# Performance work log

Measured on AMD Instinct MI355X. Metric: run time of the kernel, lower is better.

The kernel has to match this reference:

```python
import jax, jax.numpy as jnp
import numpy as np
import math

B, C, T = 4, 512, 2048
LN_EPS = 1e-5

def setup_inputs() -> dict:
    key = jax.random.key(0)
    ks = jax.random.split(key, 12)
    s = 1.0 / math.sqrt(C)
    inp = {
        'feat': jax.random.normal(ks[0], (B, C, T), dtype=jnp.float32),
        'Wq': jax.random.normal(ks[1], (C, C), dtype=jnp.float32) * s,
        'bq': jax.random.normal(ks[2], (C,), dtype=jnp.float32) * s,
        'Wk': jax.random.normal(ks[3], (C, C), dtype=jnp.float32) * s,
        'bk': jax.random.normal(ks[4], (C,), dtype=jnp.float32) * s,
        'Wv': jax.random.normal(ks[5], (C, C), dtype=jnp.float32) * s,
        'bv': jax.random.normal(ks[6], (C,), dtype=jnp.float32) * s,
        'Ws': jax.random.normal(ks[7], (C, C), dtype=jnp.float32) * s,
        'bs': jax.random.normal(ks[8], (C,), dtype=jnp.float32) * s,
        'Wl': jax.random.normal(ks[9], (C,), dtype=jnp.float32) * s,
        'bl': jax.random.normal(ks[10], (1,), dtype=jnp.float32) * s,
    }
    return inp

def reference(feat, Wq, bq, Wk, bk, Wv, bv, Ws, bs, Wl, bl):
    d = feat.shape[1]
    # 1x1 Conv1d == per-position linear over channels. feat: [B,C,T]
    value = jnp.einsum('oc,bct->bto', Wv, feat) + bv          # [B,T,C]
    query = jnp.einsum('oc,bct->bto', Wq, feat) + bq          # [B,T,C]
    key_  = jnp.einsum('oc,bct->bct', Wk, feat) + bk[:, None] # [B,C,T]
    f = jnp.einsum('btc,bcs->bts', query, key_) / math.sqrt(d)
    f = jax.nn.softmax(f, axis=2)                             # [B,T,T]
    y = jnp.einsum('bts,bsc->btc', f, value)                  # [B,T,C]
    f_score = jax.nn.sigmoid(jnp.einsum('btc,c->bt', y, Wl) + bl[0])
    z = jnp.einsum('bts,bsc->btc', 1.0 - f, value)            # [B,T,C]
    b_score = 1.0 - jax.nn.sigmoid(jnp.einsum('btc,c->bt', z, Wl) + bl[0])
    f_score = (f_score + b_score) / 2.0
    y_ct = jnp.einsum('oc,btc->bot', Ws, y) + bs[:, None]     # smooth conv, [B,C,T]
    out = feat + y_ct
    # LayerNorm over (C, T) jointly, default affine (weight=1, bias=0)
    mu = jnp.mean(out, axis=(1, 2), keepdims=True)
    var = jnp.mean(jnp.square(out - mu), axis=(1, 2), keepdims=True)
    out = (out - mu) * jax.lax.rsqrt(var + LN_EPS)
    return out, f_score
```

## Files before the change

kernel.cpp:

```cpp
#include <hip/hip_runtime.h>
#include <hip/hip_bf16.h>

#define BB 4
#define CC 512
#define TT 2048
static constexpr long CT  = (long)CC * TT;
static constexpr long TC  = (long)TT * CC;
static constexpr long TTT = (long)TT * TT;
static constexpr float SM_SCALE = 0.04419417382415922f;

typedef __bf16 bf16;
typedef __attribute__((ext_vector_type(8))) __bf16 bf16x8;
typedef __attribute__((ext_vector_type(4))) __bf16 bf16x4;
typedef __attribute__((ext_vector_type(4))) float f32x4;

__device__ __forceinline__ void load_lds16(const bf16* g, bf16* l)
{
    __builtin_amdgcn_global_load_lds(
        (const __attribute__((address_space(1))) void*)g,
        (__attribute__((address_space(3))) void*)l, 16, 0, 0);
}

#define FENCE asm volatile("" ::: "memory")

template <int N> __device__ __forceinline__ void vm_wait()
{
    if constexpr (N == 0)       asm volatile("s_waitcnt vmcnt(0)" ::: "memory");
    else if constexpr (N == 4)  asm volatile("s_waitcnt vmcnt(4)" ::: "memory");
    else if constexpr (N == 5)  asm volatile("s_waitcnt vmcnt(5)" ::: "memory");
    else if constexpr (N == 8)  asm volatile("s_waitcnt vmcnt(8)" ::: "memory");
    else if constexpr (N == 10) asm volatile("s_waitcnt vmcnt(10)" ::: "memory");
    else static_assert(N == 0, "unsupported vmcnt literal");
}

template <int TM, int TN, int WR, int WC, int BK, int DEPTH>
struct CorePipe {
    static constexpr int THREADS = WR * WC * 64;
    static constexpr int MI = TM / (WR * 16);
    static constexpr int NI = TN / (WC * 16);
    static constexpr int CPR = BK / 8;
    static constexpr int RSH = (BK == 64) ? 3 : 2;
    static constexpr int CMASK = CPR - 1;
    static constexpr int CHUNKS = (TM + TN) * CPR;
    static constexpr int ACH = TM * CPR;
    static constexpr int CPT = CHUNKS / THREADS;
    static_assert(CPT * THREADS == CHUNKS, "chunk divisibility");
    static_assert(DEPTH == 2 || DEPTH == 3, "depth 2 or 3");

    __device__ static __forceinline__ void stage(
        const bf16* __restrict__ Ab, const bf16* __restrict__ Bb,
        int K, int m0, int n0, int t, int p, bf16* As, bf16* Bs, int tid)
    {
#pragma unroll
        for (int i = 0; i < CPT; ++i) {
            int c = tid + i * THREADS;
            if (c < ACH) {
                int row = c >> RSH;
                int gc  = (c & CMASK) ^ (row & CMASK);
                load_lds16(Ab + (long)(m0 + row) * K + t * BK + gc * 8,
                           As + p * (TM * BK) + c * 8);
            } else {
                int d = c - ACH;
                int row = d >> RSH;
                int gc  = (d & CMASK) ^ (row & CMASK);
                load_lds16(Bb + (long)(n0 + row) * K + t * BK + gc * 8,
                           Bs + p * (TN * BK) + d * 8);
            }
        }
    }

    __device__ static __forceinline__ void run(
        const bf16* __restrict__ Ab, const bf16* __restrict__ Bb,
        int K, int m0, int n0, bf16* As, bf16* Bs, f32x4 (&acc)[MI][NI])
    {
        const int tid  = threadIdx.x;
        const int lane = tid & 63;
        const int wid  = tid >> 6;
        const int wr = (wid / WC) * (MI * 16);
        const int wc = (wid % WC) * (NI * 16);
        const int lm = lane & 15;
        const int lq = lane >> 4;
        const int nt = K / BK;

#pragma unroll
        for (int d = 0; d < DEPTH; ++d)
            stage(Ab, Bb, K, m0, n0, d, d, As, Bs, tid);
        vm_wait<CPT * (DEPTH - 1)>();
        FENCE; __builtin_amdgcn_s_barrier(); FENCE;

        int p = 0;
        for (int t = 0; t < nt; ++t) {
            const bf16* Ap = As + p * (TM * BK);
            const bf16* Bp = Bs + p * (TN * BK);
            bf16x8 af[BK / 32][MI], bfr[BK / 32][NI];
#pragma unroll
            for (int ks = 0; ks < BK / 32; ++ks) {
#pragma unroll
                for (int i = 0; i < MI; ++i) {
                    int ar = wr + i * 16 + lm;
                    int cc = (ks * 4 + lq) ^ (ar & CMASK);
                    af[ks][i] = *(const bf16x8*)(Ap + ar * BK + cc * 8);
                }
#pragma unroll
                for (int i = 0; i < NI; ++i) {
                    int br = wc + i * 16 + lm;
                    int cc = (ks * 4 + lq) ^ (br & CMASK);
                    bfr[ks][i] = *(const bf16x8*)(Bp + br * BK + cc * 8);
                }
            }
            asm volatile("s_waitcnt lgkmcnt(0)" ::: "memory");
            __builtin_amdgcn_sched_barrier(0);
            FENCE; __builtin_amdgcn_s_barrier(); FENCE;
            if (t + DEPTH < nt)
                stage(Ab, Bb, K, m0, n0, t + DEPTH, p, As, Bs, tid);
            __builtin_amdgcn_s_setprio(1);
#pragma unroll
            for (int ks = 0; ks < BK / 32; ++ks)
#pragma unroll
                for (int mi = 0; mi < MI; ++mi)
#pragma unroll
                    for (int ni = 0; ni < NI; ++ni)
                        acc[mi][ni] = __builtin_amdgcn_mfma_f32_16x16x32_bf16(
                            af[ks][mi], bfr[ks][ni], acc[mi][ni], 0, 0, 0);
            __builtin_amdgcn_s_setprio(0);
            if (t + 1 < nt) {
                const int rem = nt - t;
                if (rem > DEPTH)                    vm_wait<CPT * (DEPTH - 1)>();
                else if (DEPTH == 3 && rem == 3)    vm_wait<CPT>();
                else                                vm_wait<0>();
                FENCE; __builtin_amdgcn_s_barrier(); FENCE;
            }
            p = (p + 1 == DEPTH) ? 0 : p + 1;
        }
    }
};

using CPVS  = CorePipe<128, 128, 4, 2, 64, 2>;
using CPOUT = CorePipe<64, 256, 1, 8, 64, 2>;

struct CoreQVPipe {
    static constexpr int THREADS = 512;
    static constexpr int MI = 2;
    static constexpr int NI = 4;
    static constexpr int BK = 64;
    static constexpr int CPR = 8, RSH = 3, CMASK = 7;
    static constexpr int ACH = 128 * 8;
    static constexpr int CHUNKS = 256 * 8;
    static constexpr int CPT = CHUNKS / THREADS;

    __device__ static __forceinline__ void stage(
        const bf16* __restrict__ Ab, const bf16* __restrict__ Bq,
        const bf16* __restrict__ Bv, int m0, int t, int p,
        bf16* As, bf16* Bs, int tid)
    {
#pragma unroll
        for (int i = 0; i < CPT; ++i) {
            int c = tid + i * THREADS;
            if (c < ACH) {
                int row = c >> RSH;
                int gc  = (c & CMASK) ^ (row & CMASK);
                load_lds16(Ab + (long)(m0 + row) * 512 + t * 64 + gc * 8,
                           As + p * (128 * 64) + c * 8);
            } else {
                int d = c - ACH;
                int row = d >> RSH;
                int gc  = (d & CMASK) ^ (row & CMASK);
                const bf16* src = (row < 64)
                    ? Bq + (long)row * 512
                    : Bv + (long)(row - 64) * 512;
                load_lds16(src + t * 64 + gc * 8, Bs + p * (128 * 64) + d * 8);
            }
        }
    }

    __device__ static __forceinline__ void run(
        const bf16* __restrict__ Ab, const bf16* __restrict__ Bq,
        const bf16* __restrict__ Bv,
        int m0, bf16* As, bf16* Bs, f32x4 (&acc)[MI][NI])
    {
        const int tid  = threadIdx.x;
        const int lane = tid & 63;
        const int wid  = tid >> 6;
        const int wr = (wid / 2) * 32;
        const int wc = (wid % 2) * 64;
        const int lm = lane & 15;
        const int lq = lane >> 4;
        const int nt = 8;

        stage(Ab, Bq, Bv, m0, 0, 0, As, Bs, tid);
        stage(Ab, Bq, Bv, m0, 1, 1, As, Bs, tid);
        vm_wait<4>();
        FENCE; __builtin_amdgcn_s_barrier(); FENCE;

        for (int t = 0; t < nt; ++t) {
            const int p = t & 1;
            const bf16* Ap = As + p * (128 * 64);
            const bf16* Bp = Bs + p * (128 * 64);
            bf16x8 af[2][MI], bfr[2][NI];
#pragma unroll
            for (int ks = 0; ks < 2; ++ks) {
#pragma unroll
                for (int i = 0; i < MI; ++i) {
                    int ar = wr + i * 16 + lm;
                    int cc = (ks * 4 + lq) ^ (ar & CMASK);
                    af[ks][i] = *(const bf16x8*)(Ap + ar * BK + cc * 8);
                }
#pragma unroll
                for (int i = 0; i < NI; ++i) {
                    int br = wc + i * 16 + lm;
                    int cc = (ks * 4 + lq) ^ (br & CMASK);
                    bfr[ks][i] = *(const bf16x8*)(Bp + br * BK + cc * 8);
                }
            }
            asm volatile("s_waitcnt lgkmcnt(0)" ::: "memory");
            __builtin_amdgcn_sched_barrier(0);
            FENCE; __builtin_amdgcn_s_barrier(); FENCE;
            if (t + 2 < nt)
                stage(Ab, Bq, Bv, m0, t + 2, p, As, Bs, tid);
            __builtin_amdgcn_s_setprio(1);
#pragma unroll
            for (int ks = 0; ks < 2; ++ks)
#pragma unroll
                for (int mi = 0; mi < MI; ++mi)
#pragma unroll
                    for (int ni = 0; ni < NI; ++ni)
                        acc[mi][ni] = __builtin_amdgcn_mfma_f32_16x16x32_bf16(
                            af[ks][mi], bfr[ks][ni], acc[mi][ni], 0, 0, 0);
            __builtin_amdgcn_s_setprio(0);
            if (t + 1 < nt) {
                if (t + 2 < nt) vm_wait<4>();
                else            vm_wait<0>();
                FENCE; __builtin_amdgcn_s_barrier(); FENCE;
            }
        }
    }
};

__global__ __launch_bounds__(512)
void gemm_qv_kernel(const bf16* __restrict__ featT, const bf16* __restrict__ Wq_bf,
                    const bf16* __restrict__ Wv_bf, bf16* __restrict__ Qb,
                    bf16* __restrict__ Vn, const float* __restrict__ bq,
                    const float* __restrict__ bv, const float* __restrict__ wkc,
                    const float* __restrict__ bk, float* __restrict__ qb,
                    const float* __restrict__ Wl, float* __restrict__ vl)
{
    __shared__ __align__(16) bf16 As[2 * 128 * 64];
    __shared__ __align__(16) bf16 Bs[2 * 128 * 64];
    const int rb = blockIdx.z;
    const int m0 = blockIdx.y * 128;
    const int ng = blockIdx.x;
    const long wofs = (long)(ng * 64) * 512;
    f32x4 acc[2][4] = {};
    CoreQVPipe::run(featT + (long)rb * TC, Wq_bf + wofs, Wv_bf + wofs, m0, As, Bs, acc);

    const int lane = threadIdx.x & 63, wid = threadIdx.x >> 6;
    const int wr = (wid / 2) * 32;
    const bool isV = wid & 1;
    const int lm = lane & 15, lq = lane >> 4;

    if (isV) {
        bf16* outV = Vn + (long)rb * TC;
        float* vlb = vl + (long)rb * TT;
        float vs_[2][4] = {};
#pragma unroll
        for (int mi = 0; mi < 2; ++mi)
#pragma unroll
            for (int ni = 0; ni < 4; ++ni) {
                int n = ng * 64 + ni * 16 + lm;
                float bn = bv[n], wn = Wl[n];
#pragma unroll
                for (int r = 0; r < 4; ++r) {
                    int m = m0 + wr + mi * 16 + lq * 4 + r;
                    float v = acc[mi][ni][r] + bn;
                    outV[(long)m * 512 + n] = (bf16)v;
                    vs_[mi][r] += v * wn;
                }
            }
#pragma unroll
        for (int mi = 0; mi < 2; ++mi)
#pragma unroll
            for (int r = 0; r < 4; ++r) {
                float s = vs_[mi][r];
                s += __shfl_xor(s, 1, 64); s += __shfl_xor(s, 2, 64);
                s += __shfl_xor(s, 4, 64); s += __shfl_xor(s, 8, 64);
                if (lm == 0)
                    atomicAdd(vlb + m0 + wr + mi * 16 + lq * 4 + r, s);
            }
    } else {
        bf16* out = Qb + (long)rb * TC;
        float* qbb = qb + (long)rb * TT;
        float rs[2][4] = {};
#pragma unroll
        for (int mi = 0; mi < 2; ++mi)
#pragma unroll
            for (int ni = 0; ni < 4; ++ni) {
                int n = ng * 64 + ni * 16 + lm;
                float bn = bq[n], wn = wkc[n], kn = bk[n];
#pragma unroll
                for (int r = 0; r < 4; ++r) {
                    int m = m0 + wr + mi * 16 + lq * 4 + r;
                    float v = acc[mi][ni][r] + bn;
                    rs[mi][r] += v * kn;
                    out[(long)m * 512 + n] = (bf16)(v * wn);
                }
            }
#pragma unroll
        for (int mi = 0; mi < 2; ++mi)
#pragma unroll
            for (int r = 0; r < 4; ++r) {
                float s = rs[mi][r];
                s += __shfl_xor(s, 1, 64); s += __shfl_xor(s, 2, 64);
                s += __shfl_xor(s, 4, 64); s += __shfl_xor(s, 8, 64);
                if (lm == 0)
                    atomicAdd(qbb + m0 + wr + mi * 16 + lq * 4 + r, s);
            }
    }
}

__global__ __launch_bounds__(512, 2)
void gemm_mid_kernel(const bf16* __restrict__ Qb, const bf16* __restrict__ featT,
                     bf16* __restrict__ S, const float* __restrict__ qb,
                     float* __restrict__ rsum, const float* __restrict__ vl,
                     float* __restrict__ u, const bf16* __restrict__ Vn,
                     const bf16* __restrict__ Ws_bf, bf16* __restrict__ Vpt)
{
    __shared__ __align__(16) bf16 lds[2][2][256 * 64];
    const int tid  = threadIdx.x;
    const int lane = tid & 63;
    const int wid  = tid >> 6;
    const int lm = lane & 15, lq = lane >> 4;

    if (blockIdx.x >= 256) {
        const int id2 = blockIdx.x - 256;
        const int xcd = id2 & 7, s = id2 >> 3;
        const int bz = xcd >> 1;
        const int m0 = (((xcd & 1) << 1) + (s >> 4)) * 128;
        const int n0 = (s & 15) * 128;
        bf16* As = &lds[0][0][0];
        bf16* Bs = &lds[0][1][0];
        f32x4 acc[2][4] = {};
        CPVS::run(Ws_bf, Vn + (long)bz * TC, 512, m0, n0, As, Bs, acc);

        const int wr = (wid / 2) * 32, wc = (wid % 2) * 64;
        bf16* outp = Vpt + (long)bz * CT;
#pragma unroll
        for (int mi = 0; mi < 2; ++mi)
#pragma unroll
            for (int ni = 0; ni < 4; ++ni) {
                int n = n0 + wc + ni * 16 + lm;
#pragma unroll
                for (int r = 0; r < 4; ++r) {
                    int m = m0 + wr + mi * 16 + lq * 4 + r;
                    outp[(long)m * 2048 + n] = (bf16)acc[mi][ni][r];
                }
            }
        return;
    }

    const int id   = blockIdx.x;
    const int xcd  = id & 7, sIdx = id >> 3;
    const int bz   = xcd >> 1;
    const int n0   = (sIdx & 7) * 256;
    const int m0   = (((xcd & 1) << 2) + (sIdx >> 3)) * 256;
    const bf16* __restrict__ Ab = Qb + (long)bz * TC;
    const bf16* __restrict__ Bb = featT + (long)bz * TC;

    const int wrb = (wid >> 2) * 64;
    const int wcb = (wid & 3) * 32;

    f32x4 acc[8][4] = {};

#define STAGE_HT(t, op, h)                                                    \
    do {                                                                      \
        const bf16* gp_ = (op) ? Bb : Ab;                                     \
        const int  br_  = ((op) ? n0 : m0) + (h) * 128;                       \
        bf16* lp_ = &lds[(t) & 1][op][(h) * 128 * 64];                        \
        _Pragma("unroll")                                                     \
        for (int i_ = 0; i_ < 2; ++i_) {                                      \
            int c_ = tid + i_ * 512;                                          \
            int r_ = c_ >> 3;                                                 \
            int g_ = (c_ & 7) ^ (r_ & 7);                                     \
            load_lds16(gp_ + (long)(br_ + r_) * 512 + (t) * 64 + g_ * 8,      \
                       lp_ + c_ * 8);                                         \
        }                                                                     \
    } while (0)

#define PHASE(t, qm, qn, doSt, st, sop, sh, doVm)                             \
    do {                                                                      \
        bf16x8 af[2][4], bfr[2][2];                                           \
        const bf16* Al_ = lds[(t) & 1][0];                                    \
        const bf16* Bl_ = lds[(t) & 1][1];                                    \
        _Pragma("unroll")                                                     \
        for (int ks = 0; ks < 2; ++ks) {                                      \
            _Pragma("unroll")                                                 \
            for (int j = 0; j < 4; ++j) {                                     \
                int ar = (qm) * 128 + wrb + j * 16 + lm;                      \
                int cc = (ks * 4 + lq) ^ (ar & 7);                            \
                af[ks][j] = *(const bf16x8*)(Al_ + ar * 64 + cc * 8);         \
            }                                                                 \
            _Pragma("unroll")                                                 \
            for (int j = 0; j < 2; ++j) {                                     \
                int br = (qn) * 128 + wcb + j * 16 + lm;                      \
                int cc = (ks * 4 + lq) ^ (br & 7);                            \
                bfr[ks][j] = *(const bf16x8*)(Bl_ + br * 64 + cc * 8);        \
            }                                                                 \
        }                                                                     \
        if (doSt) STAGE_HT(st, sop, sh);                                      \
        if (doVm) {                                                           \
            if ((t) < 6) asm volatile("s_waitcnt vmcnt(4)" ::: "memory");     \
            else         asm volatile("s_waitcnt vmcnt(0)" ::: "memory");     \
        }                                                                     \
        FENCE; __builtin_amdgcn_s_barrier(); FENCE;                           \
        __builtin_amdgcn_s_setprio(1);                                        \
        _Pragma("unroll")                                                     \
        for (int ks = 0; ks < 2; ++ks)                                        \
            _Pragma("unroll")                                                 \
            for (int j = 0; j < 4; ++j)                                       \
                _Pragma("unroll")                                             \
                for (int j2 = 0; j2 < 2; ++j2)                                \
                    acc[(qm) * 4 + j][(qn) * 2 + j2] =                        \
                        __builtin_amdgcn_mfma_f32_16x16x32_bf16(              \
                            af[ks][j], bfr[ks][j2],                           \
                            acc[(qm) * 4 + j][(qn) * 2 + j2], 0, 0, 0);       \
        __builtin_amdgcn_s_setprio(0);                                        \
        FENCE; __builtin_amdgcn_s_barrier(); FENCE;                           \
    } while (0)

    STAGE_HT(0, 0, 0); STAGE_HT(0, 1, 0); STAGE_HT(0, 0, 1); STAGE_HT(0, 1, 1);
    STAGE_HT(1, 0, 0); STAGE_HT(1, 1, 0);
    asm volatile("s_waitcnt vmcnt(4)" ::: "memory");
    FENCE; __builtin_amdgcn_s_barrier(); FENCE;

    for (int t = 0; t < 8; ++t) {
        PHASE(t, 0, 0, t + 1 < 8, t + 1, 0, 1, false);
        PHASE(t, 0, 1, t + 1 < 8, t + 1, 1, 1, false);
        PHASE(t, 1, 0, t + 2 < 8, t + 2, 0, 0, false);
        PHASE(t, 1, 1, t + 2 < 8, t + 2, 1, 0, true);
    }
#undef PHASE
#undef STAGE_HT

    bf16* outp = S + (long)bz * TTT;
    const float* qbb = qb + (long)bz * TT;
    const float* vlb = vl + (long)bz * TT;
    float* rsb = rsum + (long)bz * TT;
    float* ub  = u + (long)bz * TT;
#pragma unroll
    for (int mi = 0; mi < 8; ++mi) {
        const int mrow = m0 + (mi >> 2) * 128 + wrb + (mi & 3) * 16 + lq * 4;
        const f32x4 qv = *(const f32x4*)(qbb + mrow);
        float rp[4] = {0.f, 0.f, 0.f, 0.f};
        float up[4] = {0.f, 0.f, 0.f, 0.f};
#pragma unroll
        for (int ni = 0; ni < 4; ++ni) {
            const int ncol = n0 + (ni >> 1) * 128 + wcb + (ni & 1) * 16 + lm;
            const float vlv = vlb[ncol];
#pragma unroll
            for (int r = 0; r < 4; ++r) {
                float p = __expf((acc[mi][ni][r] + qv[r]) * SM_SCALE);
                outp[(long)(mrow + r) * 2048 + ncol] = (bf16)p;
                rp[r] += p;
                up[r] += p * vlv;
            }
        }
#pragma unroll
        for (int r = 0; r < 4; ++r) {
            float s2 = rp[r], s3 = up[r];
            s2 += __shfl_xor(s2, 1, 64); s2 += __shfl_xor(s2, 2, 64);
            s2 += __shfl_xor(s2, 4, 64); s2 += __shfl_xor(s2, 8, 64);
            s3 += __shfl_xor(s3, 1, 64); s3 += __shfl_xor(s3, 2, 64);
            s3 += __shfl_xor(s3, 4, 64); s3 += __shfl_xor(s3, 8, 64);
            if (lm == 0) {
                atomicAdd(rsb + mrow + r, s2);
                atomicAdd(ub + mrow + r, s3);
            }
        }
    }
}

__global__ __launch_bounds__(512)
void gemm_out_kernel(const bf16* __restrict__ S, const bf16* __restrict__ Vpt,
                     float* __restrict__ out, const float* __restrict__ bs,
                     const float* __restrict__ feat,
                     const float* __restrict__ rsum, double* __restrict__ stats)
{
    __shared__ __align__(16) bf16 As[2 * 64 * 64];
    __shared__ __align__(16) bf16 Bs[2 * 256 * 64];
    __shared__ float red[16];
    const int id = blockIdx.x;
    const int xcd = id & 7, sIdx = id >> 3;
    const int bz = xcd >> 1;
    const int n0 = (sIdx & 1) * 256;
    const int m0 = (((xcd & 1) << 4) + (sIdx >> 1)) * 64;
    f32x4 acc[4][2] = {};
    CPOUT::run(S + (long)bz * TTT, Vpt + (long)bz * CT, 2048, m0, n0, As, Bs, acc);

    const int tid = threadIdx.x;
    const int lane = tid & 63, wid = tid >> 6;
    const int lm = lane & 15, lq = lane >> 4;
    const float* rsb = rsum + (long)bz * TT;
    float inv[4][4];
#pragma unroll
    for (int mi = 0; mi < 4; ++mi) {
        int mrow = m0 + mi * 16 + lq * 4;
        f32x4 rv = *(const f32x4*)(rsb + mrow);
#pragma unroll
        for (int r = 0; r < 4; ++r) inv[mi][r] = 1.f / rv[r];
    }
    float s1 = 0.f, s2 = 0.f;
#pragma unroll
    for (int mi = 0; mi < 4; ++mi)
#pragma unroll
        for (int ni = 0; ni < 2; ++ni) {
            int mrow = m0 + mi * 16 + lq * 4;
            int n = n0 + wid * 32 + ni * 16 + lm;
            long off = (long)bz * CT + (long)n * TT + mrow;
            f32x4 fv = *(const f32x4*)(feat + off);
            float bn = bs[n];
            f32x4 res;
#pragma unroll
            for (int r = 0; r < 4; ++r) {
                float v = acc[mi][ni][r] * inv[mi][r] + bn + fv[r];
                res[r] = v;
                s1 += v;
                s2 += v * v;
            }
            *(f32x4*)(out + off) = res;
        }
#pragma unroll
    for (int off = 32; off; off >>= 1) {
        s1 += __shfl_xor(s1, off, 64);
        s2 += __shfl_xor(s2, off, 64);
    }
    if (lane == 0) { red[wid] = s1; red[8 + wid] = s2; }
    __syncthreads();
    if (tid == 0) {
        double t1 = 0.0, t2 = 0.0;
#pragma unroll
        for (int w = 0; w < 8; ++w) { t1 += red[w]; t2 += red[8 + w]; }
        atomicAdd(stats + bz * 2, t1);
        atomicAdd(stats + bz * 2 + 1, t2);
    }
}

__global__ __launch_bounds__(256)
void prep_kernel(const float* __restrict__ feat, bf16* __restrict__ featT,
                 const float* __restrict__ Wq, const float* __restrict__ Wv,
                 const float* __restrict__ Ws, bf16* __restrict__ Wbf,
                 const float* __restrict__ Wk, const float* __restrict__ Wl,
                 const float* __restrict__ bv, float* __restrict__ wkc,
                 float* __restrict__ wvl, float* __restrict__ wlbv,
                 float* __restrict__ frp, float* __restrict__ qb,
                 float* __restrict__ u, float* __restrict__ rsum,
                 double* __restrict__ stats, float* __restrict__ vl)
{
    const int blk = blockIdx.x;
    const int tid = threadIdx.x;
    if (blk < 4096) {
        __shared__ float tile[32][33];
        __shared__ float sfr[4][32];
        const int b  = blk >> 10;
        const int c0 = ((blk & 1023) >> 6) * 32;
        const int tt = blk & 63;
        const int t0 = tt * 32;
        const int tx = tid & 31;
        const int ty = tid >> 5;
#pragma unroll
        for (int j = 0; j < 4; ++j) {
            int c = c0 + ty + j * 8;
            tile[ty + j * 8][tx] = feat[(long)b * CT + (long)c * TT + t0 + tx];
        }
        __syncthreads();
        float ps = 0.f;
#pragma unroll
        for (int j = 0; j < 4; ++j) {
            int tl = ty + j * 8;
            int t = t0 + tl;
            int c = c0 + tx;
            float v = tile[tx][tl];
            ps += v;
            featT[(long)b * TC + (long)t * CC + c] = (bf16)v;
        }
        const int wid = tid >> 6;
        ps += __shfl_xor(ps, 32, 64);
        if ((tid & 63) < 32) sfr[wid][tx] = ps;
        __syncthreads();
        if (tid < 32) {
            float s = sfr[0][tid] + sfr[1][tid] + sfr[2][tid] + sfr[3][tid];
            frp[(((long)b * 64 + tt) << 9) + c0 + tid] = s;
        }
    } else if (blk < 4480) {
        long gid = (long)(blk - 4096) * 256 + tid;
        long idx = gid * 8;
        int w = (int)(idx >> 18);
        long off = idx & 262143;
        const float* src = (w == 0) ? Wq : (w == 1) ? Wv : Ws;
        f32x4 a = *(const f32x4*)(src + off);
        f32x4 b = *(const f32x4*)(src + off + 4);
        bf16x8 o;
#pragma unroll
        for (int j = 0; j < 4; ++j) { o[j] = (bf16)a[j]; o[4 + j] = (bf16)b[j]; }
        *(bf16x8*)(Wbf + idx) = o;
    } else {
        int mid = (blk - 4480) * 256 + tid;
        if (mid < 512) {
            float s = 0.f;
            for (int o = 0; o < 512; ++o) s += Wk[o * 512 + mid];
            wkc[mid] = s;
        } else if (mid < 1024) {
            int k = mid - 512;
            float s = 0.f;
            for (int c = 0; c < 512; ++c) s += Wl[c] * Wv[c * 512 + k];
            wvl[k] = s;
        } else if (mid < 1088) {
            int lane = mid - 1024;
            float s = 0.f;
#pragma unroll
            for (int j = 0; j < 8; ++j) s += Wl[lane + 64 * j] * bv[lane + 64 * j];
#pragma unroll
            for (int off = 32; off; off >>= 1) s += __shfl_xor(s, off, 64);
            if (lane == 0) wlbv[0] = s;
        } else if (mid >= 1152 && mid < 1160) {
            stats[mid - 1152] = 0.0;
        } else if (mid >= 4096 && mid < 12288) {
            qb[mid - 4096] = 0.f;
        } else if (mid >= 12288 && mid < 20480) {
            u[mid - 12288] = 0.f;
        } else if (mid >= 20480 && mid < 28672) {
            rsum[mid - 20480] = 0.f;
        } else if (mid >= 28672 && mid < 36864) {
            vl[mid - 28672] = 0.f;
        }
    }
}

__global__ __launch_bounds__(256)
void ln_score_kernel(float* __restrict__ out, const double* __restrict__ stats,
                     const float* __restrict__ u, const float* __restrict__ frp,
                     const float* __restrict__ wvl, const float* __restrict__ wlbv,
                     const float* __restrict__ blp, const float* __restrict__ rsum)
{
    if (blockIdx.x < 4096) {
        long i = ((long)blockIdx.x * 256 + threadIdx.x) * 4;
        int b = (int)(i >> 20);
        const double n = 1048576.0;
        double mu  = stats[b * 2] / n;
        double var = stats[b * 2 + 1] / n - mu * mu;
        float rs = (float)(1.0 / sqrt(var + 1e-5));
        float muf = (float)mu;
        f32x4 v = *(f32x4*)(out + i);
#pragma unroll
        for (int j = 0; j < 4; ++j) v[j] = (v[j] - muf) * rs;
        *(f32x4*)(out + i) = v;
    } else {
        const int b = blockIdx.x - 4096;
        __shared__ float ssv[4];
        const int tid = threadIdx.x, lane = tid & 63, wid = tid >> 6;
        const float* fb = frp + ((long)b * 64 << 9);
        float s0 = 0.f, s1 = 0.f;
#pragma unroll 8
        for (int k = 0; k < 64; ++k) {
            s0 += fb[(k << 9) + tid];
            s1 += fb[(k << 9) + tid + 256];
        }
        float p = s0 * wvl[tid] + s1 * wvl[tid + 256];
#pragma unroll
        for (int off = 32; off; off >>= 1) p += __shfl_xor(p, off, 64);
        if (lane == 0) ssv[wid] = p;
        __syncthreads();
        const float sv = ssv[0] + ssv[1] + ssv[2] + ssv[3] + 2048.f * wlbv[0];
        const float bl0 = blp[0];
#pragma unroll
        for (int j = 0; j < 8; ++j) {
            int t = tid + j * 256;
            float uu = u[(long)b * TT + t] / rsum[(long)b * TT + t];
            float uf = uu + bl0;
            float vf = sv - uu + bl0;
            float fs  = 1.f / (1.f + __expf(-uf));
            float bsc = 1.f - 1.f / (1.f + __expf(-vf));
            out[(long)BB * CT + (long)b * TT + t] = 0.5f * (fs + bsc);
        }
    }
}

extern "C" void kernel_launch(void* const* d_in, const int* in_sizes, int n_in,
                              void* d_out, int out_size, void* d_ws, size_t ws_size,
                              hipStream_t stream)
{
    const float* feat = (const float*)d_in[0];
    const float* Wq   = (const float*)d_in[1];
    const float* bq   = (const float*)d_in[2];
    const float* Wk   = (const float*)d_in[3];
    const float* bk   = (const float*)d_in[4];
    const float* Wv   = (const float*)d_in[5];
    const float* bv   = (const float*)d_in[6];
    const float* Ws   = (const float*)d_in[7];
    const float* bs   = (const float*)d_in[8];
    const float* Wl   = (const float*)d_in[9];
    const float* bl   = (const float*)d_in[10];
    float* out = (float*)d_out;

    if (ws_size < 69349504) return;
    char* ws = (char*)d_ws;
    bf16* featT  = (bf16*)(ws);
    bf16* Wbf    = (bf16*)(ws + 8388608);
    bf16* Qb     = (bf16*)(ws + 9961472);
    bf16* Vn     = (bf16*)(ws + 18350080);
    bf16* Vpt    = (bf16*)(ws + 26738688);
    bf16* S      = (bf16*)(ws + 35127296);
    float* wkc   = (float*)(ws + 68689920);
    float* wvl   = (float*)(ws + 68691968);
    float* wlbv  = (float*)(ws + 68694016);
    float* qb    = (float*)(ws + 68694080);
    double* stats= (double*)(ws + 68726848);
    float* u     = (float*)(ws + 68726912);
    float* rsum  = (float*)(ws + 68759680);
    float* frp   = (float*)(ws + 68792448);
    float* vl    = (float*)(ws + 69316736);

    bf16* Wq_bf = Wbf;
    bf16* Wv_bf = Wbf + 262144;
    bf16* Ws_bf = Wbf + 524288;

    prep_kernel<<<4624, 256, 0, stream>>>(feat, featT, Wq, Wv, Ws, Wbf, Wk, Wl, bv,
                                          wkc, wvl, wlbv, frp, qb, u, rsum, stats, vl);
    gemm_qv_kernel<<<dim3(8, 16, 4), 512, 0, stream>>>(
        featT, Wq_bf, Wv_bf, Qb, Vn, bq, bv, wkc, bk, qb, Wl, vl);
    gemm_mid_kernel<<<512, 512, 0, stream>>>(Qb, featT, S, qb, rsum, vl, u,
                                             Vn, Ws_bf, Vpt);
    gemm_out_kernel<<<256, 512, 0, stream>>>(S, Vpt, out, bs, feat, rsum, stats);
    ln_score_kernel<<<4100, 256, 0, stream>>>(out, stats, u, frp, wvl, wlbv, bl, rsum);
}
```

Baseline: 212.1 us.

## Fold Ws into Wv so V projection directly yields Ws·V, dropping the per-batch GEMM

Precomputes the weight product Ws·Wv (and bias Ws·bv) in a small new kernel, so the QV projection writes the smoothed value tensor Vpt directly instead of producing V and then running a separate Ws×V GEMM per batch inside the middle kernel. The vl vector (Wl·V) is now computed from featT with the precomputed Wl·Wv vector instead of atomics in the QV epilogue. This removes a batch-sized GEMM and the V intermediate at the cost of an extra launch and an extra bf16 rounding of the fused weight.

```diff
diff --git a/kernel.cpp b/kernel.cpp
--- a/kernel.cpp
+++ b/kernel.cpp
@@ -25,27 +25,25 @@
 
 template <int N> __device__ __forceinline__ void vm_wait()
 {
-    if constexpr (N == 0)       asm volatile("s_waitcnt vmcnt(0)" ::: "memory");
-    else if constexpr (N == 4)  asm volatile("s_waitcnt vmcnt(4)" ::: "memory");
-    else if constexpr (N == 5)  asm volatile("s_waitcnt vmcnt(5)" ::: "memory");
-    else if constexpr (N == 8)  asm volatile("s_waitcnt vmcnt(8)" ::: "memory");
-    else if constexpr (N == 10) asm volatile("s_waitcnt vmcnt(10)" ::: "memory");
+    if constexpr (N == 0)      asm volatile("s_waitcnt vmcnt(0)" ::: "memory");
+    else if constexpr (N == 3) asm volatile("s_waitcnt vmcnt(3)" ::: "memory");
+    else if constexpr (N == 4) asm volatile("s_waitcnt vmcnt(4)" ::: "memory");
+    else if constexpr (N == 5) asm volatile("s_waitcnt vmcnt(5)" ::: "memory");
     else static_assert(N == 0, "unsupported vmcnt literal");
 }
 
-template <int TM, int TN, int WR, int WC, int BK, int DEPTH>
+template <int TM, int TN, int WR, int WC, int BK>
 struct CorePipe {
     static constexpr int THREADS = WR * WC * 64;
     static constexpr int MI = TM / (WR * 16);
     static constexpr int NI = TN / (WC * 16);
     static constexpr int CPR = BK / 8;
-    static constexpr int RSH = (BK == 64) ? 3 : 2;
+    static constexpr int RSH = 3;
     static constexpr int CMASK = CPR - 1;
     static constexpr int CHUNKS = (TM + TN) * CPR;
     static constexpr int ACH = TM * CPR;
     static constexpr int CPT = CHUNKS / THREADS;
     static_assert(CPT * THREADS == CHUNKS, "chunk divisibility");
-    static_assert(DEPTH == 2 || DEPTH == 3, "depth 2 or 3");
 
     __device__ static __forceinline__ void stage(
         const bf16* __restrict__ Ab, const bf16* __restrict__ Bb,
@@ -82,14 +80,13 @@
         const int lq = lane >> 4;
         const int nt = K / BK;
 
-#pragma unroll
-        for (int d = 0; d < DEPTH; ++d)
-            stage(Ab, Bb, K, m0, n0, d, d, As, Bs, tid);
-        vm_wait<CPT * (DEPTH - 1)>();
+        stage(Ab, Bb, K, m0, n0, 0, 0, As, Bs, tid);
+        stage(Ab, Bb, K, m0, n0, 1, 1, As, Bs, tid);
+        vm_wait<CPT>();
         FENCE; __builtin_amdgcn_s_barrier(); FENCE;
 
-        int p = 0;
         for (int t = 0; t < nt; ++t) {
+            const int p = t & 1;
             const bf16* Ap = As + p * (TM * BK);
             const bf16* Bp = Bs + p * (TN * BK);
             bf16x8 af[BK / 32][MI], bfr[BK / 32][NI];
@@ -111,8 +108,8 @@
             asm volatile("s_waitcnt lgkmcnt(0)" ::: "memory");
             __builtin_amdgcn_sched_barrier(0);
             FENCE; __builtin_amdgcn_s_barrier(); FENCE;
-            if (t + DEPTH < nt)
-                stage(Ab, Bb, K, m0, n0, t + DEPTH, p, As, Bs, tid);
+            if (t + 2 < nt)
+                stage(Ab, Bb, K, m0, n0, t + 2, p, As, Bs, tid);
             __builtin_amdgcn_s_setprio(1);
 #pragma unroll
             for (int ks = 0; ks < BK / 32; ++ks)
@@ -124,29 +121,19 @@
                             af[ks][mi], bfr[ks][ni], acc[mi][ni], 0, 0, 0);
             __builtin_amdgcn_s_setprio(0);
             if (t + 1 < nt) {
-                const int rem = nt - t;
-                if (rem > DEPTH)                    vm_wait<CPT * (DEPTH - 1)>();
-                else if (DEPTH == 3 && rem == 3)    vm_wait<CPT>();
-                else                                vm_wait<0>();
+                if (t + 2 < nt) vm_wait<CPT>();
+                else            vm_wait<0>();
                 FENCE; __builtin_amdgcn_s_barrier(); FENCE;
             }
-            p = (p + 1 == DEPTH) ? 0 : p + 1;
         }
     }
 };
 
-using CPVS  = CorePipe<128, 128, 4, 2, 64, 2>;
-using CPOUT = CorePipe<64, 256, 1, 8, 64, 2>;
+using CW    = CorePipe<128, 64, 4, 2, 64>;
+using CPOUT = CorePipe<64, 256, 1, 8, 64>;
 
 struct CoreQVPipe {
-    static constexpr int THREADS = 512;
-    static constexpr int MI = 2;
-    static constexpr int NI = 4;
-    static constexpr int BK = 64;
-    static constexpr int CPR = 8, RSH = 3, CMASK = 7;
     static constexpr int ACH = 128 * 8;
-    static constexpr int CHUNKS = 256 * 8;
-    static constexpr int CPT = CHUNKS / THREADS;
 
     __device__ static __forceinline__ void stage(
         const bf16* __restrict__ Ab, const bf16* __restrict__ Bq,
@@ -154,17 +141,17 @@
         bf16* As, bf16* Bs, int tid)
     {
 #pragma unroll
-        for (int i = 0; i < CPT; ++i) {
-            int c = tid + i * THREADS;
+        for (int i = 0; i < 4; ++i) {
+            int c = tid + i * 512;
             if (c < ACH) {
-                int row = c >> RSH;
-                int gc  = (c & CMASK) ^ (row & CMASK);
+                int row = c >> 3;
+                int gc  = (c & 7) ^ (row & 7);
                 load_lds16(Ab + (long)(m0 + row) * 512 + t * 64 + gc * 8,
                            As + p * (128 * 64) + c * 8);
             } else {
                 int d = c - ACH;
-                int row = d >> RSH;
-                int gc  = (d & CMASK) ^ (row & CMASK);
+                int row = d >> 3;
+                int gc  = (d & 7) ^ (row & 7);
                 const bf16* src = (row < 64)
                     ? Bq + (long)row * 512
                     : Bv + (long)(row - 64) * 512;
@@ -176,7 +163,7 @@
     __device__ static __forceinline__ void run(
         const bf16* __restrict__ Ab, const bf16* __restrict__ Bq,
         const bf16* __restrict__ Bv,
-        int m0, bf16* As, bf16* Bs, f32x4 (&acc)[MI][NI])
+        int m0, bf16* As, bf16* Bs, f32x4 (&acc)[2][4])
     {
         const int tid  = threadIdx.x;
         const int lane = tid & 63;
@@ -196,20 +183,20 @@
             const int p = t & 1;
             const bf16* Ap = As + p * (128 * 64);
             const bf16* Bp = Bs + p * (128 * 64);
-            bf16x8 af[2][MI], bfr[2][NI];
+            bf16x8 af[2][2], bfr[2][4];
 #pragma unroll
             for (int ks = 0; ks < 2; ++ks) {
 #pragma unroll
-                for (int i = 0; i < MI; ++i) {
+                for (int i = 0; i < 2; ++i) {
                     int ar = wr + i * 16 + lm;
-                    int cc = (ks * 4 + lq) ^ (ar & CMASK);
-                    af[ks][i] = *(const bf16x8*)(Ap + ar * BK + cc * 8);
+                    int cc = (ks * 4 + lq) ^ (ar & 7);
+                    af[ks][i] = *(const bf16x8*)(Ap + ar * 64 + cc * 8);
                 }
 #pragma unroll
-                for (int i = 0; i < NI; ++i) {
+                for (int i = 0; i < 4; ++i) {
                     int br = wc + i * 16 + lm;
-                    int cc = (ks * 4 + lq) ^ (br & CMASK);
-                    bfr[ks][i] = *(const bf16x8*)(Bp + br * BK + cc * 8);
+                    int cc = (ks * 4 + lq) ^ (br & 7);
+                    bfr[ks][i] = *(const bf16x8*)(Bp + br * 64 + cc * 8);
                 }
             }
             asm volatile("s_waitcnt lgkmcnt(0)" ::: "memory");
@@ -221,9 +208,9 @@
 #pragma unroll
             for (int ks = 0; ks < 2; ++ks)
 #pragma unroll
-                for (int mi = 0; mi < MI; ++mi)
-#pragma unroll
-                    for (int ni = 0; ni < NI; ++ni)
+                for (int mi = 0; mi < 2; ++mi)
+#pragma unroll
+                    for (int ni = 0; ni < 4; ++ni)
                         acc[mi][ni] = __builtin_amdgcn_mfma_f32_16x16x32_bf16(
                             af[ks][mi], bfr[ks][ni], acc[mi][ni], 0, 0, 0);
             __builtin_amdgcn_s_setprio(0);
@@ -238,11 +225,10 @@
 
 __global__ __launch_bounds__(512)
 void gemm_qv_kernel(const bf16* __restrict__ featT, const bf16* __restrict__ Wq_bf,
-                    const bf16* __restrict__ Wv_bf, bf16* __restrict__ Qb,
-                    bf16* __restrict__ Vn, const float* __restrict__ bq,
-                    const float* __restrict__ bv, const float* __restrict__ wkc,
-                    const float* __restrict__ bk, float* __restrict__ qb,
-                    const float* __restrict__ Wl, float* __restrict__ vl)
+                    const bf16* __restrict__ Wsv_bf, bf16* __restrict__ Qb,
+                    bf16* __restrict__ Vpt, const float* __restrict__ bq,
+                    const float* __restrict__ bsv, const float* __restrict__ wkc,
+                    const float* __restrict__ bk, float* __restrict__ qb)
 {
     __shared__ __align__(16) bf16 As[2 * 128 * 64];
     __shared__ __align__(16) bf16 Bs[2 * 128 * 64];
@@ -251,7 +237,7 @@
     const int ng = blockIdx.x;
     const long wofs = (long)(ng * 64) * 512;
     f32x4 acc[2][4] = {};
-    CoreQVPipe::run(featT + (long)rb * TC, Wq_bf + wofs, Wv_bf + wofs, m0, As, Bs, acc);
+    CoreQVPipe::run(featT + (long)rb * TC, Wq_bf + wofs, Wsv_bf + wofs, m0, As, Bs, acc);
 
     const int lane = threadIdx.x & 63, wid = threadIdx.x >> 6;
     const int wr = (wid / 2) * 32;
@@ -259,32 +245,18 @@
     const int lm = lane & 15, lq = lane >> 4;
 
     if (isV) {
-        bf16* outV = Vn + (long)rb * TC;
-        float* vlb = vl + (long)rb * TT;
-        float vs_[2][4] = {};
+        bf16* outV = Vpt + (long)rb * CT;
 #pragma unroll
         for (int mi = 0; mi < 2; ++mi)
 #pragma unroll
             for (int ni = 0; ni < 4; ++ni) {
                 int n = ng * 64 + ni * 16 + lm;
-                float bn = bv[n], wn = Wl[n];
-#pragma unroll
-                for (int r = 0; r < 4; ++r) {
-                    int m = m0 + wr + mi * 16 + lq * 4 + r;
-                    float v = acc[mi][ni][r] + bn;
-                    outV[(long)m * 512 + n] = (bf16)v;
-                    vs_[mi][r] += v * wn;
-                }
-            }
-#pragma unroll
-        for (int mi = 0; mi < 2; ++mi)
-#pragma unroll
-            for (int r = 0; r < 4; ++r) {
-                float s = vs_[mi][r];
-                s += __shfl_xor(s, 1, 64); s += __shfl_xor(s, 2, 64);
-                s += __shfl_xor(s, 4, 64); s += __shfl_xor(s, 8, 64);
-                if (lm == 0)
-                    atomicAdd(vlb + m0 + wr + mi * 16 + lq * 4 + r, s);
+                float bn = bsv[n];
+                int mb = m0 + wr + mi * 16 + lq * 4;
+                bf16x4 pk;
+#pragma unroll
+                for (int r = 0; r < 4; ++r) pk[r] = (bf16)(acc[mi][ni][r] + bn);
+                *(bf16x4*)(outV + (long)n * TT + mb) = pk;
             }
     } else {
         bf16* out = Qb + (long)rb * TC;
@@ -317,46 +289,61 @@
     }
 }
 
-__global__ __launch_bounds__(512, 2)
-void gemm_mid_kernel(const bf16* __restrict__ Qb, const bf16* __restrict__ featT,
-                     bf16* __restrict__ S, const float* __restrict__ qb,
-                     float* __restrict__ rsum, const float* __restrict__ vl,
-                     float* __restrict__ u, const bf16* __restrict__ Vn,
-                     const bf16* __restrict__ Ws_bf, bf16* __restrict__ Vpt)
-{
-    __shared__ __align__(16) bf16 lds[2][2][256 * 64];
-    const int tid  = threadIdx.x;
-    const int lane = tid & 63;
-    const int wid  = tid >> 6;
-    const int lm = lane & 15, lq = lane >> 4;
-
-    if (blockIdx.x >= 256) {
-        const int id2 = blockIdx.x - 256;
-        const int xcd = id2 & 7, s = id2 >> 3;
-        const int bz = xcd >> 1;
-        const int m0 = (((xcd & 1) << 1) + (s >> 4)) * 128;
-        const int n0 = (s & 15) * 128;
-        bf16* As = &lds[0][0][0];
-        bf16* Bs = &lds[0][1][0];
-        f32x4 acc[2][4] = {};
-        CPVS::run(Ws_bf, Vn + (long)bz * TC, 512, m0, n0, As, Bs, acc);
-
-        const int wr = (wid / 2) * 32, wc = (wid % 2) * 64;
-        bf16* outp = Vpt + (long)bz * CT;
+__global__ __launch_bounds__(512)
+void wsv_kernel(const bf16* __restrict__ Ws_bf, const bf16* __restrict__ WvT_bf,
+                bf16* __restrict__ Wsv_bf, const bf16* __restrict__ featT,
+                const float* __restrict__ wvl, const float* __restrict__ wlbv,
+                float* __restrict__ vl)
+{
+    __shared__ __align__(16) bf16 As[2 * 128 * 64];
+    __shared__ __align__(16) bf16 Bs[2 * 64 * 64];
+    const int tid = threadIdx.x;
+    const int lane = tid & 63, wid = tid >> 6;
+
+    if (blockIdx.x < 32) {
+        const int m0 = (blockIdx.x & 3) * 128;
+        const int n0 = (blockIdx.x >> 2) * 64;
+        f32x4 acc[2][2] = {};
+        CW::run(Ws_bf, WvT_bf, 512, m0, n0, As, Bs, acc);
+        const int wr = (wid / 2) * 32, wc = (wid % 2) * 32;
+        const int lm = lane & 15, lq = lane >> 4;
 #pragma unroll
         for (int mi = 0; mi < 2; ++mi)
 #pragma unroll
-            for (int ni = 0; ni < 4; ++ni) {
+            for (int ni = 0; ni < 2; ++ni) {
                 int n = n0 + wc + ni * 16 + lm;
 #pragma unroll
                 for (int r = 0; r < 4; ++r) {
                     int m = m0 + wr + mi * 16 + lq * 4 + r;
-                    outp[(long)m * 2048 + n] = (bf16)acc[mi][ni][r];
+                    Wsv_bf[(long)m * 512 + n] = (bf16)acc[mi][ni][r];
                 }
             }
-        return;
-    }
-
+    } else {
+        float wv8[8];
+#pragma unroll
+        for (int j = 0; j < 8; ++j) wv8[j] = wvl[lane * 8 + j];
+        const float w0 = wlbv[0];
+        const int r0 = (blockIdx.x - 32) * 256 + wid * 32;
+        for (int rr = 0; rr < 32; ++rr) {
+            int row = r0 + rr;
+            bf16x8 v = *(const bf16x8*)(featT + (long)row * 512 + lane * 8);
+            float s = 0.f;
+#pragma unroll
+            for (int j = 0; j < 8; ++j) s += (float)v[j] * wv8[j];
+#pragma unroll
+            for (int off = 32; off; off >>= 1) s += __shfl_xor(s, off, 64);
+            if (lane == 0) vl[row] = s + w0;
+        }
+    }
+}
+
+__global__ __launch_bounds__(512, 2)
+void gemm_s256_kernel(const bf16* __restrict__ Qb, const bf16* __restrict__ featT,
+                      bf16* __restrict__ S, const float* __restrict__ qb,
+                      float* __restrict__ rsum, const float* __restrict__ vl,
+                      float* __restrict__ u)
+{
+    __shared__ __align__(16) bf16 lds[2][2][256 * 64];
     const int id   = blockIdx.x;
     const int xcd  = id & 7, sIdx = id >> 3;
     const int bz   = xcd >> 1;
@@ -365,6 +352,10 @@
     const bf16* __restrict__ Ab = Qb + (long)bz * TC;
     const bf16* __restrict__ Bb = featT + (long)bz * TC;
 
+    const int tid  = threadIdx.x;
+    const int lane = tid & 63;
+    const int wid  = tid >> 6;
+    const int lm = lane & 15, lq = lane >> 4;
     const int wrb = (wid >> 2) * 64;
     const int wcb = (wid & 3) * 32;
 
@@ -552,7 +543,7 @@
                  float* __restrict__ wvl, float* __restrict__ wlbv,
                  float* __restrict__ frp, float* __restrict__ qb,
                  float* __restrict__ u, float* __restrict__ rsum,
-                 double* __restrict__ stats, float* __restrict__ vl)
+                 double* __restrict__ stats, float* __restrict__ bsv)
 {
     const int blk = blockIdx.x;
     const int tid = threadIdx.x;
@@ -589,20 +580,37 @@
             float s = sfr[0][tid] + sfr[1][tid] + sfr[2][tid] + sfr[3][tid];
             frp[(((long)b * 64 + tt) << 9) + c0 + tid] = s;
         }
-    } else if (blk < 4480) {
+    } else if (blk < 4352) {
         long gid = (long)(blk - 4096) * 256 + tid;
         long idx = gid * 8;
         int w = (int)(idx >> 18);
         long off = idx & 262143;
-        const float* src = (w == 0) ? Wq : (w == 1) ? Wv : Ws;
+        const float* src = (w == 0) ? Wq : Ws;
         f32x4 a = *(const f32x4*)(src + off);
         f32x4 b = *(const f32x4*)(src + off + 4);
         bf16x8 o;
 #pragma unroll
         for (int j = 0; j < 4; ++j) { o[j] = (bf16)a[j]; o[4 + j] = (bf16)b[j]; }
         *(bf16x8*)(Wbf + idx) = o;
+    } else if (blk < 4608) {
+        __shared__ float tile[32][33];
+        const int blk2 = blk - 4352;
+        const int c0 = (blk2 >> 4) * 32;
+        const int o0 = (blk2 & 15) * 32;
+        const int tx = tid & 31;
+        const int ty = tid >> 5;
+        bf16* WvT = Wbf + 524288;
+#pragma unroll
+        for (int j = 0; j < 4; ++j)
+            tile[ty + j * 8][tx] = Wv[(long)(c0 + ty + j * 8) * 512 + o0 + tx];
+        __syncthreads();
+#pragma unroll
+        for (int j = 0; j < 4; ++j) {
+            int ol = ty + j * 8;
+            WvT[(long)(o0 + ol) * 512 + c0 + tx] = (bf16)tile[tx][ol];
+        }
     } else {
-        int mid = (blk - 4480) * 256 + tid;
+        int mid = (blk - 4608) * 256 + tid;
         if (mid < 512) {
             float s = 0.f;
             for (int o = 0; o < 512; ++o) s += Wk[o * 512 + mid];
@@ -620,16 +628,19 @@
 #pragma unroll
             for (int off = 32; off; off >>= 1) s += __shfl_xor(s, off, 64);
             if (lane == 0) wlbv[0] = s;
-        } else if (mid >= 1152 && mid < 1160) {
-            stats[mid - 1152] = 0.0;
+        } else if (mid >= 1536 && mid < 2048) {
+            int j = mid - 1536;
+            float s = 0.f;
+            for (int c = 0; c < 512; ++c) s += Ws[(long)j * 512 + c] * bv[c];
+            bsv[j] = s;
+        } else if (mid >= 3072 && mid < 3080) {
+            stats[mid - 3072] = 0.0;
         } else if (mid >= 4096 && mid < 12288) {
             qb[mid - 4096] = 0.f;
         } else if (mid >= 12288 && mid < 20480) {
             u[mid - 12288] = 0.f;
         } else if (mid >= 20480 && mid < 28672) {
             rsum[mid - 20480] = 0.f;
-        } else if (mid >= 28672 && mid < 36864) {
-            vl[mid - 28672] = 0.f;
         }
     }
 }
@@ -705,7 +716,8 @@
     bf16* featT  = (bf16*)(ws);
     bf16* Wbf    = (bf16*)(ws + 8388608);
     bf16* Qb     = (bf16*)(ws + 9961472);
-    bf16* Vn     = (bf16*)(ws + 18350080);
+    bf16* Wsv_bf = (bf16*)(ws + 18350080);
+    float* bsv   = (float*)(ws + 18874368);
     bf16* Vpt    = (bf16*)(ws + 26738688);
     bf16* S      = (bf16*)(ws + 35127296);
     float* wkc   = (float*)(ws + 68689920);
@@ -718,16 +730,17 @@
     float* frp   = (float*)(ws + 68792448);
     float* vl    = (float*)(ws + 69316736);
 
-    bf16* Wq_bf = Wbf;
-    bf16* Wv_bf = Wbf + 262144;
-    bf16* Ws_bf = Wbf + 524288;
-
-    prep_kernel<<<4624, 256, 0, stream>>>(feat, featT, Wq, Wv, Ws, Wbf, Wk, Wl, bv,
-                                          wkc, wvl, wlbv, frp, qb, u, rsum, stats, vl);
+    bf16* Wq_bf  = Wbf;
+    bf16* Ws_bf  = Wbf + 262144;
+    bf16* WvT_bf = Wbf + 524288;
+
+    prep_kernel<<<4720, 256, 0, stream>>>(feat, featT, Wq, Wv, Ws, Wbf, Wk, Wl, bv,
+                                          wkc, wvl, wlbv, frp, qb, u, rsum, stats,
+                                          bsv);
+    wsv_kernel<<<64, 512, 0, stream>>>(Ws_bf, WvT_bf, Wsv_bf, featT, wvl, wlbv, vl);
     gemm_qv_kernel<<<dim3(8, 16, 4), 512, 0, stream>>>(
-        featT, Wq_bf, Wv_bf, Qb, Vn, bq, bv, wkc, bk, qb, Wl, vl);
-    gemm_mid_kernel<<<512, 512, 0, stream>>>(Qb, featT, S, qb, rsum, vl, u,
-                                             Vn, Ws_bf, Vpt);
+        featT, Wq_bf, Wsv_bf, Qb, Vpt, bq, bsv, wkc, bk, qb);
+    gemm_s256_kernel<<<256, 512, 0, stream>>>(Qb, featT, S, qb, rsum, vl, u);
     gemm_out_kernel<<<256, 512, 0, stream>>>(S, Vpt, out, bs, feat, rsum, stats);
     ln_score_kernel<<<4100, 256, 0, stream>>>(out, stats, u, frp, wvl, wlbv, bl, rsum);
 }
```

Result: slower. 224.1 us (+5.6%).
